# Performance work log

Hardware: AMD Instinct MI355X
Metric: run time of the kernel (lower is better)

Reference implementation:

```python
import jax, jax.numpy as jnp
import numpy as np

D = 1024
H = 16
DH = D // H
LN_EPS = 1e-5


def setup_inputs() -> dict:
    key = jax.random.key(0)
    ks = jax.random.split(key, 8)
    B, L = 32768, 3
    q = jax.random.normal(ks[0], (B, 1, D), dtype=jnp.float32)
    x = jax.random.normal(ks[1], (B, L, D), dtype=jnp.float32)
    s = 0.02  # weight init scale
    Wq = jax.random.normal(ks[2], (D, D), dtype=jnp.float32) * s
    Wk = jax.random.normal(ks[3], (D, D), dtype=jnp.float32) * s
    Wv = jax.random.normal(ks[4], (D, D), dtype=jnp.float32) * s
    Wr = jax.random.normal(ks[5], (D, D), dtype=jnp.float32) * s
    Wo = jax.random.normal(ks[6], (D, D), dtype=jnp.float32) * s
    ln_gamma = jnp.ones((D,), dtype=jnp.float32)
    ln_beta = jnp.zeros((D,), dtype=jnp.float32)
    return {"q": q, "x": x, "Wq": Wq, "Wk": Wk, "Wv": Wv, "Wr": Wr,
            "Wo": Wo, "ln_gamma": ln_gamma, "ln_beta": ln_beta}


def _layer_norm(y, gamma, beta):
    mu = jnp.mean(y, axis=-1, keepdims=True)
    var = jnp.mean(jnp.square(y - mu), axis=-1, keepdims=True)
    return (y - mu) * jax.lax.rsqrt(var + LN_EPS) * gamma + beta


def reference(q, x, Wq, Wk, Wv, Wr, Wo, ln_gamma, ln_beta):
    # torch Linear(no bias): y = inp @ W^T
    Q = jnp.einsum('bqd,ed->bqe', q, Wq)            # [B,1,D]
    K = jnp.einsum('bld,ed->ble', x, Wk)            # [B,L,D]
    V = jnp.einsum('bld,ed->ble', x, Wv)
    R = jnp.einsum('bld,ed->ble', x, Wr)
    V_eff = jax.nn.sigmoid(R) * V                   # gated V
    B, L = x.shape[0], x.shape[1]
    Qh = Q.reshape(B, 1, H, DH).transpose(0, 2, 1, 3)   # [B,H,1,Dh]
    Kh = K.reshape(B, L, H, DH).transpose(0, 2, 1, 3)   # [B,H,L,Dh]
    Vh = V_eff.reshape(B, L, H, DH).transpose(0, 2, 1, 3)
    scores = jnp.einsum('bhqd,bhld->bhql', Qh, Kh) / jnp.sqrt(jnp.float32(DH))
    attn = jax.nn.softmax(scores, axis=-1)              # [B,H,1,L]; dropout=eval no-op
    out = jnp.einsum('bhql,bhld->bhqd', attn, Vh)       # [B,H,1,Dh]
    out = out.transpose(0, 2, 1, 3).reshape(B, 1, D)
    out = jnp.einsum('bqd,ed->bqe', out, Wo)
    out = _layer_norm(q + out, ln_gamma, ln_beta)
    return out, attn
```

## Files before the change

### kernel.cpp

```cpp
#include <hip/hip_runtime.h>
#include <math.h>


using half8   = __attribute__((ext_vector_type(8))) _Float16;
using half4   = __attribute__((ext_vector_type(4))) _Float16;
using floatx4 = __attribute__((ext_vector_type(4))) float;

#define BTOT 32768
#define DM   1024
#define NH   16
#define LSEQ 3

__device__ __forceinline__ void gload_lds16(const void* g, void* l) {
  __builtin_amdgcn_global_load_lds(
      (const __attribute__((address_space(1))) void*)g,
      (__attribute__((address_space(3))) void*)l, 16, 0, 0);
}

#define WAITVM(N) do { __builtin_amdgcn_sched_barrier(0);            \
  asm volatile("s_waitcnt vmcnt(" #N ")" ::: "memory");              \
  __builtin_amdgcn_sched_barrier(0); } while (0)

__global__ __launch_bounds__(256) void acvt(
    const float* __restrict__ xc, _Float16* __restrict__ x16,
    const float* __restrict__ qc, _Float16* __restrict__ q16, int xblocks)
{
  const int blk = blockIdx.x;
  const float* src;
  _Float16* dst;
  size_t o;
  if (blk < xblocks) {
    o = ((size_t)blk * 256 + threadIdx.x) * 4;
    src = xc; dst = x16;
  } else {
    o = ((size_t)(blk - xblocks) * 256 + threadIdx.x) * 4;
    src = qc; dst = q16;
  }
  floatx4 a = *(const floatx4*)(src + o);
  half4 h;
  h[0] = (_Float16)a[0]; h[1] = (_Float16)a[1];
  h[2] = (_Float16)a[2]; h[3] = (_Float16)a[3];
  *(half4*)(dst + o) = h;
}

__global__ __launch_bounds__(256) void wconv(
    const float* __restrict__ Wq, const float* __restrict__ Wk,
    const float* __restrict__ Wv, const float* __restrict__ Wr,
    const float* __restrict__ Wo,
    _Float16* __restrict__ Wq16, _Float16* __restrict__ Wkvr16,
    _Float16* __restrict__ Wo16)
{
  const int i = blockIdx.x * 256 + threadIdx.x;
  const size_t o = (size_t)i * 4;
  const size_t M1 = (size_t)1024 * 1024;
  floatx4 a;
  half4 h;
#define CVT(SRC, DST, OFF)                                        \
  a = *(const floatx4*)((SRC) + o);                               \
  h[0] = (_Float16)a[0]; h[1] = (_Float16)a[1];                   \
  h[2] = (_Float16)a[2]; h[3] = (_Float16)a[3];                   \
  *(half4*)((DST) + (OFF) + o) = h;
  CVT(Wq, Wq16, 0)
  CVT(Wo, Wo16, 0)
  CVT(Wk, Wkvr16, 0)
  CVT(Wv, Wkvr16, M1)
  CVT(Wr, Wkvr16, 2 * M1)
#undef CVT
}

template <bool OUT_HALF>
__global__ __launch_bounds__(256) void gemm_bt(
    const _Float16* __restrict__ A, const _Float16* __restrict__ Bw,
    void* __restrict__ Cout, int M, int N, int K)
{
  __shared__ __attribute__((aligned(16))) char As[128 * 128];
  __shared__ __attribute__((aligned(16))) char Bs[128 * 128];

  const int tid  = threadIdx.x;
  const int lane = tid & 63;
  const int wave = tid >> 6;
  const int wr = wave >> 1, wc = wave & 1;
  const int l15 = lane & 15, lk = lane >> 4;

  const int nwg = gridDim.x * gridDim.y;
  int wgid = blockIdx.y * gridDim.x + blockIdx.x;
  wgid = (wgid & 7) * (nwg >> 3) + (wgid >> 3);
  const int bx = wgid % gridDim.x;
  const int by = wgid / gridDim.x;

  const int col0 = bx * 128;
  const int row0 = by * 128;

  floatx4 acc[4][4] = {};

  const int nK = K >> 6;
  for (int kt = 0; kt < nK; ++kt) {
    const int k0 = kt << 6;
    {
      const char* gA = (const char*)A + ((size_t)row0 * K + k0) * 2;
      const char* gB = (const char*)Bw + ((size_t)col0 * K + k0) * 2;
      #pragma unroll
      for (int it = 0; it < 4; ++it) {
        const int off = it * 4096 + tid * 16;
        const int row = off >> 7;
        const int ch  = (off >> 4) & 7;
        const int sch = ch ^ (row & 7);
        gload_lds16(gA + (size_t)row * ((size_t)K * 2) + (sch << 4), As + off);
        gload_lds16(gB + (size_t)row * ((size_t)K * 2) + (sch << 4), Bs + off);
      }
    }
    __syncthreads();
    #pragma unroll
    for (int kk = 0; kk < 64; kk += 32) {
      half8 af[4], bf[4];
      const int c = (kk >> 3) + lk;
      #pragma unroll
      for (int m = 0; m < 4; ++m) {
        const int rw = wr * 64 + m * 16 + l15;
        af[m] = *(const half8*)(As + rw * 128 + ((c ^ (rw & 7)) << 4));
      }
      #pragma unroll
      for (int n = 0; n < 4; ++n) {
        const int rw = wc * 64 + n * 16 + l15;
        bf[n] = *(const half8*)(Bs + rw * 128 + ((c ^ (rw & 7)) << 4));
      }
      #pragma unroll
      for (int m = 0; m < 4; ++m)
        #pragma unroll
        for (int n = 0; n < 4; ++n)
          acc[m][n] = __builtin_amdgcn_mfma_f32_16x16x32_f16(
              af[m], bf[n], acc[m][n], 0, 0, 0);
    }
    __syncthreads();
  }
  #pragma unroll
  for (int m = 0; m < 4; ++m) {
    const int rbase = row0 + wr * 64 + m * 16 + (lk << 2);
    #pragma unroll
    for (int r = 0; r < 4; ++r) {
      const size_t rowoff = (size_t)(rbase + r) * N;
      #pragma unroll
      for (int n = 0; n < 4; ++n) {
        const int col = col0 + wc * 64 + n * 16 + l15;
        const float v = acc[m][n][r];
        if constexpr (OUT_HALF)
          ((_Float16*)Cout)[rowoff + col] = (_Float16)v;
        else
          ((float*)Cout)[rowoff + col] = v;
      }
    }
  }
}

template <int BUF, int CK, int MH, bool LOADB, typename SF, typename GF>
__device__ __forceinline__ void phase(const char* ldsp, int aoff, int boff,
                                      int ca0, int ca1,
                                      half8 (&bf)[4], floatx4 (&acc)[8][4],
                                      SF&& stage, GF&& gate)
{
  const int ca = CK ? ca1 : ca0;
  half8 af[4];
  #pragma unroll
  for (int m = 0; m < 4; ++m)
    af[m] = *(const half8*)(ldsp + BUF * 32768 + aoff + (MH * 4 + m) * 2048 + ca);
  if constexpr (LOADB) {
    #pragma unroll
    for (int n = 0; n < 4; ++n)
      bf[n] = *(const half8*)(ldsp + 65536 + BUF * 32768 + boff + n * 2048 + ca);
  }
  stage();
  gate();
  __builtin_amdgcn_s_barrier();
  __builtin_amdgcn_s_setprio(1);
  #pragma unroll
  for (int m = 0; m < 4; ++m)
    #pragma unroll
    for (int n = 0; n < 4; ++n)
      acc[MH * 4 + m][n] = __builtin_amdgcn_mfma_f32_16x16x32_f16(
          af[m], bf[n], acc[MH * 4 + m][n], 0, 0, 0);
  __builtin_amdgcn_s_setprio(0);
  __builtin_amdgcn_s_barrier();
}

template <bool OUT_HALF>
__global__ __launch_bounds__(512, 2) void gemm256(
    const _Float16* __restrict__ A, const _Float16* __restrict__ Bw,
    void* __restrict__ Cout, int M, int N, int K)
{
  __shared__ __attribute__((aligned(16))) char lds[131072];
  const int tid  = threadIdx.x;
  const int lane = tid & 63;
  const int wave = tid >> 6;
  const int wm = wave >> 2, wn = wave & 3;
  const int l15 = lane & 15, lk = lane >> 4;
  const int sx = l15 & 7;

  const int nwg = gridDim.x * gridDim.y;
  int wgid = blockIdx.y * gridDim.x + blockIdx.x;
  wgid = (wgid & 7) * (nwg >> 3) + (wgid >> 3);
  const int bx = wgid % gridDim.x;
  const int by = wgid / gridDim.x;
  const int col0 = bx * 256, row0 = by * 256;

  const size_t Kb = (size_t)K * 2;
  const char* gA = (const char*)A + (size_t)row0 * Kb;
  const char* gB = (const char*)Bw + (size_t)col0 * Kb;
  char* ldsc = (char*)lds;

  auto stA = [&](int buf, int half, int kt) {
    #pragma unroll
    for (int ld = 0; ld < 2; ++ld) {
      const int off = ld * 8192 + tid * 16;
      const int r = off >> 7;
      const int sch = ((off >> 4) & 7) ^ (r & 7);
      gload_lds16(gA + (size_t)(half * 128 + r) * Kb + kt * 128 + (sch << 4),
                  ldsc + buf * 32768 + half * 16384 + off);
    }
  };
  auto stB = [&](int buf, int half, int kt) {
    #pragma unroll
    for (int ld = 0; ld < 2; ++ld) {
      const int off = ld * 8192 + tid * 16;
      const int r = off >> 7;
      const int sch = ((off >> 4) & 7) ^ (r & 7);
      gload_lds16(gB + (size_t)(half * 128 + r) * Kb + kt * 128 + (sch << 4),
                  ldsc + 65536 + buf * 32768 + half * 16384 + off);
    }
  };

  const int aoff = (wm * 128 + l15) * 128;
  const int boff = (wn * 64 + l15) * 128;
  const int ca0 = (lk ^ sx) << 4;
  const int ca1 = ((4 + lk) ^ sx) << 4;

  floatx4 acc[8][4] = {};
  half8 bf[4];

  stA(0, 0, 0); stA(0, 1, 0); stB(0, 0, 0); stB(0, 1, 0);
  stB(1, 0, 1);
  WAITVM(2);
  __builtin_amdgcn_s_barrier();

  const int nIt = K >> 7;
  for (int it = 0; it < nIt; ++it) {
    const int t1 = 2 * it + 1, t2 = 2 * it + 2, t3 = 2 * it + 3;
    const bool lastit = (it == nIt - 1);
    auto g0 = [&] {};
    auto g2 = [&] { if (!lastit) { WAITVM(2); } else { WAITVM(0); } };
    phase<0, 0, 0, true >(ldsc, aoff, boff, ca0, ca1, bf, acc,
                          [&] { stA(1, 0, t1); }, g0);
    phase<0, 0, 1, false>(ldsc, aoff, boff, ca0, ca1, bf, acc,
                          [&] { stA(1, 1, t1); }, g0);
    phase<0, 1, 0, true >(ldsc, aoff, boff, ca0, ca1, bf, acc,
                          [&] { stB(1, 1, t1); }, g0);
    phase<0, 1, 1, false>(ldsc, aoff, boff, ca0, ca1, bf, acc,
                          [&] { if (!lastit) stB(0, 0, t2); }, g2);
    phase<1, 0, 0, true >(ldsc, aoff, boff, ca0, ca1, bf, acc,
                          [&] { if (!lastit) stA(0, 0, t2); }, g0);
    phase<1, 0, 1, false>(ldsc, aoff, boff, ca0, ca1, bf, acc,
                          [&] { if (!lastit) stA(0, 1, t2); }, g0);
    phase<1, 1, 0, true >(ldsc, aoff, boff, ca0, ca1, bf, acc,
                          [&] { if (!lastit) stB(0, 1, t2); }, g0);
    phase<1, 1, 1, false>(ldsc, aoff, boff, ca0, ca1, bf, acc,
                          [&] { if (!lastit) stB(1, 0, t3); }, g2);
  }

  #pragma unroll
  for (int m = 0; m < 8; ++m) {
    const int rbase = row0 + wm * 128 + m * 16 + (lk << 2);
    #pragma unroll
    for (int r = 0; r < 4; ++r) {
      const size_t rowoff = (size_t)(rbase + r) * N;
      #pragma unroll
      for (int n = 0; n < 4; ++n) {
        const int col = col0 + wn * 64 + n * 16 + l15;
        const float v = acc[m][n][r];
        if constexpr (OUT_HALF)
          ((_Float16*)Cout)[rowoff + col] = (_Float16)v;
        else
          ((float*)Cout)[rowoff + col] = v;
      }
    }
  }
}

__global__ __launch_bounds__(256) void attn_kernel(
    const _Float16* __restrict__ Q16, const _Float16* __restrict__ KVR,
    _Float16* __restrict__ AV16, float* __restrict__ attn_out,
    size_t batch0)
{
  const int lane = threadIdx.x & 63;
  const int wave = threadIdx.x >> 6;
  const size_t b = (size_t)blockIdx.x * 4 + wave;
  const int h = lane >> 2, p = lane & 3;
  const int doff = h * 64 + p * 16;

  float qv[16];
  {
    const half8* qp = (const half8*)(Q16 + b * 1024 + doff);
    half8 q0 = qp[0], q1 = qp[1];
    #pragma unroll
    for (int i = 0; i < 8; ++i) { qv[i] = (float)q0[i]; qv[8 + i] = (float)q1[i]; }
  }
  float sc[LSEQ];
  #pragma unroll
  for (int l = 0; l < LSEQ; ++l) {
    const half8* kp = (const half8*)(KVR + (b * 3 + l) * 3072 + doff);
    half8 k0 = kp[0], k1 = kp[1];
    float d = 0.f;
    #pragma unroll
    for (int i = 0; i < 8; ++i)
      d += qv[i] * (float)k0[i] + qv[8 + i] * (float)k1[i];
    d += __shfl_xor(d, 1);
    d += __shfl_xor(d, 2);
    sc[l] = d * 0.125f;
  }
  const float mx = fmaxf(sc[0], fmaxf(sc[1], sc[2]));
  const float e0 = __expf(sc[0] - mx), e1 = __expf(sc[1] - mx),
              e2 = __expf(sc[2] - mx);
  const float inv = 1.f / (e0 + e1 + e2);
  const float at0 = e0 * inv, at1 = e1 * inv, at2 = e2 * inv;
  if (p == 0) {
    float* ao = attn_out + ((batch0 + b) * NH + h) * LSEQ;
    ao[0] = at0; ao[1] = at1; ao[2] = at2;
  }
  const float atw[LSEQ] = {at0, at1, at2};
  float av[16] = {};
  #pragma unroll
  for (int l = 0; l < LSEQ; ++l) {
    const half8* vp = (const half8*)(KVR + (b * 3 + l) * 3072 + 1024 + doff);
    const half8* rp = (const half8*)(KVR + (b * 3 + l) * 3072 + 2048 + doff);
    half8 v0 = vp[0], v1 = vp[1], r0 = rp[0], r1 = rp[1];
    #pragma unroll
    for (int i = 0; i < 8; ++i) {
      const float g0 = 1.f / (1.f + __expf(-(float)r0[i]));
      const float g1 = 1.f / (1.f + __expf(-(float)r1[i]));
      av[i]     += atw[l] * g0 * (float)v0[i];
      av[8 + i] += atw[l] * g1 * (float)v1[i];
    }
  }
  half8 o0, o1;
  #pragma unroll
  for (int i = 0; i < 8; ++i) { o0[i] = (_Float16)av[i]; o1[i] = (_Float16)av[8 + i]; }
  half8* op = (half8*)(AV16 + b * 1024 + doff);
  op[0] = o0; op[1] = o1;
}

__global__ __launch_bounds__(256) void ln_kernel(
    const float* __restrict__ qres, const float* __restrict__ outlin,
    const float* __restrict__ gamma, const float* __restrict__ beta,
    float* __restrict__ out)
{
  const int lane = threadIdx.x & 63;
  const size_t r = (size_t)blockIdx.x * 4 + (threadIdx.x >> 6);
  const size_t base = r * 1024 + lane * 16;
  floatx4 y[4];
  float s = 0.f, ss = 0.f;
  #pragma unroll
  for (int i = 0; i < 4; ++i) {
    floatx4 a  = *(const floatx4*)(qres + base + i * 4);
    floatx4 bb = *(const floatx4*)(outlin + base + i * 4);
    y[i] = a + bb;
    #pragma unroll
    for (int j = 0; j < 4; ++j) { s += y[i][j]; ss += y[i][j] * y[i][j]; }
  }
  #pragma unroll
  for (int o = 1; o < 64; o <<= 1) {
    s  += __shfl_xor(s, o);
    ss += __shfl_xor(ss, o);
  }
  const float mu  = s * (1.f / 1024.f);
  const float var = ss * (1.f / 1024.f) - mu * mu;
  const float rs  = rsqrtf(var + 1e-5f);
  #pragma unroll
  for (int i = 0; i < 4; ++i) {
    floatx4 g  = *(const floatx4*)(gamma + lane * 16 + i * 4);
    floatx4 be = *(const floatx4*)(beta + lane * 16 + i * 4);
    floatx4 o;
    #pragma unroll
    for (int j = 0; j < 4; ++j)
      o[j] = (y[i][j] - mu) * rs * g[j] + be[j];
    *(floatx4*)(out + base + i * 4) = o;
  }
}

extern "C" void kernel_launch(void* const* d_in, const int* in_sizes, int n_in,
                              void* d_out, int out_size, void* d_ws, size_t ws_size,
                              hipStream_t stream)
{
  const float* q     = (const float*)d_in[0];
  const float* x     = (const float*)d_in[1];
  const float* Wq    = (const float*)d_in[2];
  const float* Wk    = (const float*)d_in[3];
  const float* Wv    = (const float*)d_in[4];
  const float* Wr    = (const float*)d_in[5];
  const float* Wo    = (const float*)d_in[6];
  const float* gamma = (const float*)d_in[7];
  const float* beta  = (const float*)d_in[8];

  float* out      = (float*)d_out;
  float* attn_out = out + (size_t)BTOT * DM;

  char* ws = (char*)d_ws;
  _Float16* Wq16   = (_Float16*)ws; ws += (size_t)1024 * 1024 * 2;
  _Float16* Wkvr16 = (_Float16*)ws; ws += (size_t)3072 * 1024 * 2;
  _Float16* Wo16   = (_Float16*)ws; ws += (size_t)1024 * 1024 * 2;

  const size_t wbytes = (size_t)10 * 1024 * 1024;
  const size_t rem = ws_size > wbytes ? ws_size - wbytes : 0;
  int CB = 128;
  for (int c = BTOT; c >= 128; c >>= 1)
    if ((size_t)c * 34816 <= rem) { CB = c; break; }

  _Float16* x16  = (_Float16*)ws; ws += (size_t)CB * 3 * 1024 * 2;
  _Float16* q16  = (_Float16*)ws; ws += (size_t)CB * 1024 * 2;
  _Float16* Q16  = (_Float16*)ws; ws += (size_t)CB * 1024 * 2;
  _Float16* KVR  = (_Float16*)ws; ws += (size_t)CB * 3 * 3072 * 2;
  _Float16* AV16 = (_Float16*)ws; ws += (size_t)CB * 1024 * 2;
  float*    OUTL = (float*)ws;

  const bool big = (CB == BTOT);

  wconv<<<dim3(1024), dim3(256), 0, stream>>>(Wq, Wk, Wv, Wr, Wo,
                                              Wq16, Wkvr16, Wo16);

  const int xblk = (CB * LSEQ * DM) / 1024;
  const int qblk = (CB * DM) / 1024;
  for (int c = 0; c < BTOT; c += CB) {
    const float* qc = q + (size_t)c * DM;
    const float* xc = x + (size_t)c * LSEQ * DM;
    acvt<<<dim3(xblk + qblk), dim3(256), 0, stream>>>(xc, x16, qc, q16, xblk);
    if (big) {
      gemm256<true><<<dim3(1024 / 256, CB / 256), dim3(512), 0, stream>>>(
          q16, Wq16, Q16, CB, 1024, 1024);
      gemm256<true><<<dim3(3072 / 256, (3 * CB) / 256), dim3(512), 0, stream>>>(
          x16, Wkvr16, KVR, 3 * CB, 3072, 1024);
    } else {
      gemm_bt<true><<<dim3(1024 / 128, CB / 128), dim3(256), 0, stream>>>(
          q16, Wq16, Q16, CB, 1024, 1024);
      gemm_bt<true><<<dim3(3072 / 128, (3 * CB) / 128), dim3(256), 0, stream>>>(
          x16, Wkvr16, KVR, 3 * CB, 3072, 1024);
    }
    attn_kernel<<<dim3(CB / 4), dim3(256), 0, stream>>>(Q16, KVR, AV16,
                                                        attn_out, (size_t)c);
    if (big) {
      gemm256<false><<<dim3(1024 / 256, CB / 256), dim3(512), 0, stream>>>(
          AV16, Wo16, OUTL, CB, 1024, 1024);
    } else {
      gemm_bt<false><<<dim3(1024 / 128, CB / 128), dim3(256), 0, stream>>>(
          AV16, Wo16, OUTL, CB, 1024, 1024);
    }
    ln_kernel<<<dim3(CB / 4), dim3(256), 0, stream>>>(qc, OUTL, gamma, beta,
                                                      out + (size_t)c * DM);
  }
}
```

Before: 1.619 ms.

## Add deeper-buffered 256x256 GEMM with triple-buffered A tiles in LDS

Adds a new 256x256-tile fp16 MFMA GEMM that uses 160KB of LDS: three A stages and two B stages, with a swizzled layout. Loads for tile t+1 (B) and t+2 (A) are interleaved between MFMA clusters, with prioritised MFMA issue, a per-stage barrier and an XCD-style workgroup remap. It replaces the previous gemm256 for all three projection GEMMs when the workspace is large and an occupancy query says the kernel can launch. The aim is to hide global-load latency better. The risks are the large LDS footprint limiting a CU to one block, and the launch bound of two blocks per CU squeezing registers for 128 accumulators.

```diff
diff --git a/kernel.cpp b/kernel.cpp
--- a/kernel.cpp
+++ b/kernel.cpp
@@ -284,6 +284,140 @@
   }
 }
 
+template <bool OUT_HALF>
+__global__ __launch_bounds__(512, 2) void gemm256d(
+    const _Float16* __restrict__ A, const _Float16* __restrict__ Bw,
+    void* __restrict__ Cout, int M, int N, int K)
+{
+  __shared__ __attribute__((aligned(16))) char lds[163840];
+  const int tid  = threadIdx.x;
+  const int lane = tid & 63;
+  const int wave = tid >> 6;
+  const int wm = wave >> 2, wn = wave & 3;
+  const int l15 = lane & 15, lk = lane >> 4;
+  const int sx = l15 & 7;
+
+  const int nwg = gridDim.x * gridDim.y;
+  int wgid = blockIdx.y * gridDim.x + blockIdx.x;
+  wgid = (wgid & 7) * (nwg >> 3) + (wgid >> 3);
+  const int bx = wgid % gridDim.x;
+  const int by = wgid / gridDim.x;
+  const int col0 = bx * 256, row0 = by * 256;
+
+  const size_t Kb = (size_t)K * 2;
+  const char* gA = (const char*)A + (size_t)row0 * Kb;
+  const char* gB = (const char*)Bw + (size_t)col0 * Kb;
+  char* ldsc = (char*)lds;
+
+  auto stA = [&](int base, int half, int kt) {
+    #pragma unroll
+    for (int ld = 0; ld < 2; ++ld) {
+      const int off = ld * 8192 + tid * 16;
+      const int r = off >> 7;
+      const int sch = ((off >> 4) & 7) ^ (r & 7);
+      gload_lds16(gA + (size_t)(half * 128 + r) * Kb + kt * 128 + (sch << 4),
+                  ldsc + base + half * 16384 + off);
+    }
+  };
+  auto stB = [&](int base, int half, int kt) {
+    #pragma unroll
+    for (int ld = 0; ld < 2; ++ld) {
+      const int off = ld * 8192 + tid * 16;
+      const int r = off >> 7;
+      const int sch = ((off >> 4) & 7) ^ (r & 7);
+      gload_lds16(gB + (size_t)(half * 128 + r) * Kb + kt * 128 + (sch << 4),
+                  ldsc + base + half * 16384 + off);
+    }
+  };
+
+  const int aoff = (wm * 128 + l15) * 128;
+  const int boff = (wn * 64 + l15) * 128;
+  const int ca0 = (lk ^ sx) << 4;
+  const int ca1 = ((4 + lk) ^ sx) << 4;
+
+  floatx4 acc[8][4] = {};
+  half8 af[4], bf[4];
+
+#define MFMA_CLUSTER(MH)                                                   \
+  __builtin_amdgcn_s_barrier();                                            \
+  __builtin_amdgcn_s_setprio(1);                                           \
+  _Pragma("unroll")                                                        \
+  for (int m = 0; m < 4; ++m) {                                            \
+    _Pragma("unroll")                                                      \
+    for (int n = 0; n < 4; ++n)                                            \
+      acc[(MH) * 4 + m][n] = __builtin_amdgcn_mfma_f32_16x16x32_f16(       \
+          af[m], bf[n], acc[(MH) * 4 + m][n], 0, 0, 0);                    \
+  }                                                                        \
+  __builtin_amdgcn_s_setprio(0);
+
+  int aR = 0, aM = 32768, aS = 65536;
+  int bR = 98304, bS = 131072;
+
+  stA(aR, 0, 0); stA(aR, 1, 0);
+  stB(bR, 0, 0); stB(bR, 1, 0);
+  stA(aM, 0, 1); stA(aM, 1, 1);
+  WAITVM(4);
+  __builtin_amdgcn_s_barrier();
+
+  const int nK = K >> 6;
+  for (int t = 0; t < nK; ++t) {
+    const bool sB  = (t + 1 < nK);
+    const bool sA2 = (t + 2 < nK);
+    #pragma unroll
+    for (int m = 0; m < 4; ++m)
+      af[m] = *(const half8*)(ldsc + aR + aoff + m * 2048 + ca0);
+    #pragma unroll
+    for (int n = 0; n < 4; ++n)
+      bf[n] = *(const half8*)(ldsc + bR + boff + n * 2048 + ca0);
+    if (sB) stB(bS, 0, t + 1);
+    MFMA_CLUSTER(0)
+    __builtin_amdgcn_s_barrier();
+    #pragma unroll
+    for (int m = 0; m < 4; ++m)
+      af[m] = *(const half8*)(ldsc + aR + aoff + (4 + m) * 2048 + ca0);
+    if (sB) stB(bS, 1, t + 1);
+    MFMA_CLUSTER(1)
+    __builtin_amdgcn_s_barrier();
+    #pragma unroll
+    for (int m = 0; m < 4; ++m)
+      af[m] = *(const half8*)(ldsc + aR + aoff + m * 2048 + ca1);
+    #pragma unroll
+    for (int n = 0; n < 4; ++n)
+      bf[n] = *(const half8*)(ldsc + bR + boff + n * 2048 + ca1);
+    if (sA2) stA(aS, 0, t + 2);
+    MFMA_CLUSTER(0)
+    __builtin_amdgcn_s_barrier();
+    #pragma unroll
+    for (int m = 0; m < 4; ++m)
+      af[m] = *(const half8*)(ldsc + aR + aoff + (4 + m) * 2048 + ca1);
+    if (sA2) stA(aS, 1, t + 2);
+    MFMA_CLUSTER(1)
+    if (sB) { if (sA2) { WAITVM(4); } else { WAITVM(0); } }
+    __builtin_amdgcn_s_barrier();
+    const int ta = aR; aR = aM; aM = aS; aS = ta;
+    const int tb = bR; bR = bS; bS = tb;
+  }
+#undef MFMA_CLUSTER
+
+  #pragma unroll
+  for (int m = 0; m < 8; ++m) {
+    const int rbase = row0 + wm * 128 + m * 16 + (lk << 2);
+    #pragma unroll
+    for (int r = 0; r < 4; ++r) {
+      const size_t rowoff = (size_t)(rbase + r) * N;
+      #pragma unroll
+      for (int n = 0; n < 4; ++n) {
+        const int col = col0 + wn * 64 + n * 16 + l15;
+        const float v = acc[m][n][r];
+        if constexpr (OUT_HALF)
+          ((_Float16*)Cout)[rowoff + col] = (_Float16)v;
+        else
+          ((float*)Cout)[rowoff + col] = v;
+      }
+    }
+  }
+}
+
 __global__ __launch_bounds__(256) void attn_kernel(
     const _Float16* __restrict__ Q16, const _Float16* __restrict__ KVR,
     _Float16* __restrict__ AV16, float* __restrict__ attn_out,
@@ -421,6 +555,13 @@
 
   const bool big = (CB == BTOT);
 
+  int nb = 0;
+  if (hipOccupancyMaxActiveBlocksPerMultiprocessor(
+          &nb, reinterpret_cast<const void*>(&gemm256d<true>), 512, 0)
+      != hipSuccess)
+    nb = 0;
+  const bool deep = big && (nb > 0);
+
   wconv<<<dim3(1024), dim3(256), 0, stream>>>(Wq, Wk, Wv, Wr, Wo,
                                               Wq16, Wkvr16, Wo16);
 
@@ -430,7 +571,12 @@
     const float* qc = q + (size_t)c * DM;
     const float* xc = x + (size_t)c * LSEQ * DM;
     acvt<<<dim3(xblk + qblk), dim3(256), 0, stream>>>(xc, x16, qc, q16, xblk);
-    if (big) {
+    if (deep) {
+      gemm256d<true><<<dim3(1024 / 256, CB / 256), dim3(512), 0, stream>>>(
+          q16, Wq16, Q16, CB, 1024, 1024);
+      gemm256d<true><<<dim3(3072 / 256, (3 * CB) / 256), dim3(512), 0, stream>>>(
+          x16, Wkvr16, KVR, 3 * CB, 3072, 1024);
+    } else if (big) {
       gemm256<true><<<dim3(1024 / 256, CB / 256), dim3(512), 0, stream>>>(
           q16, Wq16, Q16, CB, 1024, 1024);
       gemm256<true><<<dim3(3072 / 256, (3 * CB) / 256), dim3(512), 0, stream>>>(
@@ -443,7 +589,10 @@
     }
     attn_kernel<<<dim3(CB / 4), dim3(256), 0, stream>>>(Q16, KVR, AV16,
                                                         attn_out, (size_t)c);
-    if (big) {
+    if (deep) {
+      gemm256d<false><<<dim3(1024 / 256, CB / 256), dim3(512), 0, stream>>>(
+          AV16, Wo16, OUTL, CB, 1024, 1024);
+    } else if (big) {
       gemm256<false><<<dim3(1024 / 256, CB / 256), dim3(512), 0, stream>>>(
           AV16, Wo16, OUTL, CB, 1024, 1024);
     } else {
```

Result: no change. 1.644 ms (+1.6%).
